# Kernel optimization log

Measured on AMD Instinct MI355X. Metric: run time of the kernel, lower is better.

Reference implementation:

```python
import jax, jax.numpy as jnp
import numpy as np

N, D, P = 8192, 512, 3
TEMP, SIM_TH, DIS_TH, CLIP = 0.1, 0.15, 0.35, 30.0
NEG = -1e9  # finite stand-in for -inf mask (exp underflows to 0 identically)


def setup_inputs() -> dict:
    key = jax.random.key(0)
    k1, k2 = jax.random.split(key)
    embeddings = jax.random.normal(k1, (N, D), dtype=jnp.float32)
    thetas = jax.random.uniform(k2, (N, P), dtype=jnp.float32)
    return {"embeddings": embeddings, "thetas": thetas}


def reference(embeddings, thetas):
    n = embeddings.shape[0]
    # F.normalize(dim=-1)
    e = embeddings / jnp.maximum(
        jnp.linalg.norm(embeddings, axis=-1, keepdims=True), 1e-12)
    sim = jnp.clip(e @ e.T / TEMP, -CLIP, CLIP)  # [N, N]

    # cdist(thetas, thetas) normalized by its max; only feeds boolean masks
    t = jax.lax.stop_gradient(thetas)
    sq = jnp.sum(t * t, axis=1)
    d2 = jnp.maximum(sq[:, None] + sq[None, :] - 2.0 * (t @ t.T), 0.0)
    dist = jnp.sqrt(d2)
    dist = dist / (dist.max() + 1e-8)

    eye = jnp.eye(n, dtype=bool)
    pos = (dist < SIM_TH) & ~eye      # positives (self excluded: diag is -inf masked)
    neg = dist > DIS_TH               # negatives (diag never included: dist==0)
    sel = pos | neg

    # per-row cross_entropy over logits [pos_idx; neg_idx] with label 0 is:
    #   -sim[i, first_pos_index(i)] + logsumexp_{j in sel(i)} sim[i, j]
    masked = jnp.where(sel, sim, NEG)
    denom = jax.nn.logsumexp(masked, axis=1)            # [N]
    tgt = jnp.argmax(pos, axis=1)                       # first positive index
    tgt_logit = jnp.take_along_axis(sim, tgt[:, None], axis=1)[:, 0]
    valid = pos.any(axis=1) & neg.any(axis=1)
    per_row = jnp.where(valid, denom - tgt_logit, 0.0)
    cnt = valid.sum()
    return jnp.where(cnt > 0, per_row.sum() / jnp.maximum(cnt, 1), 0.0)
```

## Files before the change

### kernel.cpp

```cpp
#include <hip/hip_runtime.h>

#define N 8192
#define D 512

typedef __attribute__((ext_vector_type(4))) float f32x4;
typedef __attribute__((ext_vector_type(2))) long long2v;

typedef const __attribute__((address_space(1))) unsigned int* gas_t;
typedef __attribute__((address_space(3))) unsigned int* las_t;

static __device__ __forceinline__ void gl_lds16(const void* g, char* l) {
    __builtin_amdgcn_global_load_lds((gas_t)g, (las_t)l, 16, 0, 0);
}
static __device__ __forceinline__ int tri_cum(int r) { return r * (129 - r) / 2; }

static __device__ __forceinline__ unsigned f2fp8(float f) {
    unsigned u = __float_as_uint(f);
    unsigned sgn = (u >> 24) & 0x80u;
    unsigned a = u & 0x7FFFFFFFu;
    if (a >= 0x3C800000u) {
        unsigned t = a + 0x7FFFFu + ((a >> 20) & 1u);
        unsigned code = (((t >> 23) - 120u) << 3) | ((t >> 20) & 7u);
        if (code > 0x7Eu) code = 0x7Eu;
        return sgn | code;
    }
    float af = __uint_as_float(a);
    unsigned m = (unsigned)(af * 512.0f + 0.5f);
    return sgn | (m > 8u ? 8u : m);
}
static __device__ __forceinline__ float fp82f(unsigned c) {
    unsigned e = (c >> 3) & 15u, m = c & 7u;
    float v = (e == 0u) ? (float)m * 0.001953125f
                        : __uint_as_float(((e + 120u) << 23) | (m << 20));
    return (c & 0x80u) ? -v : v;
}

__global__ void kpack(const float* __restrict__ th, float4* __restrict__ th4,
                      float* __restrict__ srow, unsigned* __restrict__ jminrow,
                      unsigned* __restrict__ negrow, unsigned* __restrict__ d2mb) {
    int i = blockIdx.x * 256 + threadIdx.x;
    if (i < N) {
        float x = th[3 * i], y = th[3 * i + 1], z = th[3 * i + 2];
        float4 v; v.x = x; v.y = y; v.z = z; v.w = x * x + y * y + z * z;
        th4[i] = v;
        srow[i] = 0.0f;
        jminrow[i] = 0xFFFFFFFFu;
        negrow[i] = 0u;
    }
    if (i == 0) *d2mb = 0u;
}

__global__ void knorm(const float* __restrict__ emb, unsigned char* __restrict__ e,
                      const float4* __restrict__ th4, unsigned* __restrict__ d2mb) {
    int w    = threadIdx.x >> 6;
    int row  = blockIdx.x * 4 + w;
    int lane = threadIdx.x & 63;
    const float4* src = (const float4*)(emb + (size_t)row * D);
    float4 v0 = src[lane * 2];
    float4 v1 = src[lane * 2 + 1];
    float ss = v0.x*v0.x + v0.y*v0.y + v0.z*v0.z + v0.w*v0.w
             + v1.x*v1.x + v1.y*v1.y + v1.z*v1.z + v1.w*v1.w;
#pragma unroll
    for (int off = 1; off < 64; off <<= 1) ss += __shfl_xor(ss, off, 64);
    float inv = 3.7982826f / fmaxf(sqrtf(ss), 1e-12f);
    unsigned c0 = f2fp8(v0.x * inv), c1 = f2fp8(v0.y * inv);
    unsigned c2 = f2fp8(v0.z * inv), c3 = f2fp8(v0.w * inv);
    unsigned c4 = f2fp8(v1.x * inv), c5 = f2fp8(v1.y * inv);
    unsigned c6 = f2fp8(v1.z * inv), c7 = f2fp8(v1.w * inv);
    uint2 pk;
    pk.x = c0 | (c1 << 8) | (c2 << 16) | (c3 << 24);
    pk.y = c4 | (c5 << 8) | (c6 << 16) | (c7 << 24);
    {
        int c = lane >> 3, u = lane & 7;
        int off8 = c * 64 + ((u < 4) ? u * 16 : (u - 4) * 16 + 8);
        *(uint2*)(e + (size_t)row * D + off8) = pk;
    }

    if (blockIdx.x < 256) {
        int widx = blockIdx.x * 4 + w;
        int q0 = widx * 4;
        int m0 = N - 4 - q0;
        float4 a0 = th4[q0], a1 = th4[q0 + 1], a2 = th4[q0 + 2], a3 = th4[q0 + 3];
        float4 b0 = th4[m0], b1 = th4[m0 + 1], b2 = th4[m0 + 2], b3 = th4[m0 + 3];
        float m = 0.0f;
        for (int j = q0 + 1 + lane; j < N; j += 64) {
            float4 tj = th4[j];
            float d;
            d = a0.w + tj.w - 2.0f * (a0.x*tj.x + a0.y*tj.y + a0.z*tj.z); m = fmaxf(m, d);
            d = a1.w + tj.w - 2.0f * (a1.x*tj.x + a1.y*tj.y + a1.z*tj.z); m = fmaxf(m, d);
            d = a2.w + tj.w - 2.0f * (a2.x*tj.x + a2.y*tj.y + a2.z*tj.z); m = fmaxf(m, d);
            d = a3.w + tj.w - 2.0f * (a3.x*tj.x + a3.y*tj.y + a3.z*tj.z); m = fmaxf(m, d);
        }
        for (int j = m0 + 1 + lane; j < N; j += 64) {
            float4 tj = th4[j];
            float d;
            d = b0.w + tj.w - 2.0f * (b0.x*tj.x + b0.y*tj.y + b0.z*tj.z); m = fmaxf(m, d);
            d = b1.w + tj.w - 2.0f * (b1.x*tj.x + b1.y*tj.y + b1.z*tj.z); m = fmaxf(m, d);
            d = b2.w + tj.w - 2.0f * (b2.x*tj.x + b2.y*tj.y + b2.z*tj.z); m = fmaxf(m, d);
            d = b3.w + tj.w - 2.0f * (b3.x*tj.x + b3.y*tj.y + b3.z*tj.z); m = fmaxf(m, d);
        }
#pragma unroll
        for (int off = 1; off < 64; off <<= 1) m = fmaxf(m, __shfl_xor(m, off, 64));
        if (lane == 0) atomicMax(d2mb, __float_as_uint(m));
    }
}

__global__ __launch_bounds__(256) void kmain(
    const unsigned char* __restrict__ e, const float4* __restrict__ th4,
    const unsigned* __restrict__ d2mb, float* __restrict__ srow,
    unsigned* __restrict__ jminrow, unsigned* __restrict__ negrow) {
    __shared__ __align__(16) char smem[32768];

    const int tid  = threadIdx.x;
    const int lane = tid & 63;
    const int w    = tid >> 6;
    const int wr   = w >> 1;
    const int wc   = w & 1;

    const int bid = (int)blockIdx.x;
    const int swz = (bid & 7) * 260 + (bid >> 3);
    int rb = (int)((129.0f - sqrtf(16641.0f - 8.0f * (float)swz)) * 0.5f);
    rb = rb < 0 ? 0 : (rb > 63 ? 63 : rb);
    while (tri_cum(rb + 1) <= swz) rb++;
    while (tri_cum(rb) > swz) rb--;
    const int cb = rb + (swz - tri_cum(rb));
    const bool isdiag = (rb == cb);
    const int r0 = rb * 128, c0 = cb * 128;

    const int ssw = (((tid & 3) ^ ((tid >> 3) & 3)) << 4);
    const unsigned char* pA0 = e + (size_t)(r0 + (tid >> 2)) * D + ssw;
    const unsigned char* pA1 = pA0 + (size_t)64 * D;
    const unsigned char* pB0 = e + (size_t)(c0 + (tid >> 2)) * D + ssw;
    const unsigned char* pB1 = pB0 + (size_t)64 * D;

    const int fr = lane & 15;
    const int fq = lane >> 4;
    const int kslot = (fq ^ ((fr >> 1) & 3)) << 4;

    f32x4 acc[4][4];
#pragma unroll
    for (int mt = 0; mt < 4; mt++)
#pragma unroll
        for (int nt = 0; nt < 4; nt++) acc[mt][nt] = (f32x4){0.f, 0.f, 0.f, 0.f};

#define STAGE(T, BUF) { \
    const int k0_ = (T) * 64; char* d_ = smem + (BUF) * 16384;   \
    gl_lds16(pA0 + k0_, d_ + tid * 16);                          \
    gl_lds16(pA1 + k0_, d_ + 4096 + tid * 16);                   \
    gl_lds16(pB0 + k0_, d_ + 8192 + tid * 16);                   \
    gl_lds16(pB1 + k0_, d_ + 12288 + tid * 16); }

#define COMPUTE(BUF) { \
    const char* cA_ = smem + (BUF) * 16384;                      \
    const char* cB_ = cA_ + 8192;                                \
    long2v a_[4], b_[4];                                         \
    _Pragma("unroll")                                            \
    for (int mt = 0; mt < 4; mt++)                               \
        a_[mt] = *(const long2v*)(cA_ + (wr * 64 + mt * 16 + fr) * 64 + kslot); \
    _Pragma("unroll")                                            \
    for (int nt = 0; nt < 4; nt++)                               \
        b_[nt] = *(const long2v*)(cB_ + (wc * 64 + nt * 16 + fr) * 64 + kslot); \
    _Pragma("unroll")                                            \
    for (int mt = 0; mt < 4; mt++)                               \
    _Pragma("unroll")                                            \
    for (int nt = 0; nt < 4; nt++) {                             \
        acc[mt][nt] = __builtin_amdgcn_mfma_f32_16x16x32_fp8_fp8( \
            a_[mt][0], b_[nt][0], acc[mt][nt], 0, 0, 0);         \
        acc[mt][nt] = __builtin_amdgcn_mfma_f32_16x16x32_fp8_fp8( \
            a_[mt][1], b_[nt][1], acc[mt][nt], 0, 0, 0);         \
    } }

#define KST(T)                                                    \
    if ((T) + 1 < 8) STAGE((T) + 1, ((T) + 1) & 1)                \
    COMPUTE((T) & 1)                                              \
    asm volatile("s_waitcnt vmcnt(0)" ::: "memory");              \
    __builtin_amdgcn_s_barrier();                                 \
    __builtin_amdgcn_sched_barrier(0);

    STAGE(0, 0)
    asm volatile("s_waitcnt vmcnt(0)" ::: "memory");
    __builtin_amdgcn_s_barrier();
    __builtin_amdgcn_sched_barrier(0);
    KST(0)  KST(1)  KST(2)  KST(3)
    KST(4)  KST(5)  KST(6)  KST(7)
#undef KST
#undef COMPUTE
#undef STAGE
    __syncthreads();

    const float dmax = sqrtf(__uint_as_float(*d2mb)) + 1e-8f;
    const float p2 = 0.0225f * dmax * dmax;
    const float n2 = 0.1225f * dmax * dmax;

    const int j0 = c0 + wc * 64 + fr;
    float4 thj[4];
#pragma unroll
    for (int nt = 0; nt < 4; nt++) thj[nt] = th4[j0 + nt * 16];

    float*    lds_rs = (float*)smem;
    unsigned* lds_rj = (unsigned*)(smem + 1024);
    unsigned* lds_rn = (unsigned*)(smem + 2048);
    float*    lds_cs = (float*)(smem + 3072);
    unsigned* lds_cj = (unsigned*)(smem + 4096);
    unsigned* lds_cn = (unsigned*)(smem + 5120);

    float    csum[4]; unsigned cjm[4], cng[4];
#pragma unroll
    for (int nt = 0; nt < 4; nt++) { csum[nt] = 0.0f; cjm[nt] = 0xFFFFFFFFu; cng[nt] = 0u; }

    const int i0 = r0 + wr * 64 + fq * 4;
#pragma unroll
    for (int mt = 0; mt < 4; mt++) {
#pragma unroll
        for (int rr = 0; rr < 4; rr++) {
            const int i = i0 + mt * 16 + rr;
            const float4 ti = th4[i];
            float sv = 0.0f; unsigned jv = 0xFFFFFFFFu, nv = 0u;
#pragma unroll
            for (int nt = 0; nt < 4; nt++) {
                const int j = j0 + nt * 16;
                const float4 tj = thj[nt];
                float dot = ti.x * tj.x + ti.y * tj.y + ti.z * tj.z;
                float d2 = fmaf(-2.0f, dot, ti.w + tj.w);
                bool pos = isdiag ? ((d2 < p2) && (j != i)) : (d2 < p2);
                bool neg = (d2 > n2);
                float c = (pos || neg) ? exp2f(acc[mt][nt][rr]) : 0.0f;
                sv += c;
                if (neg) nv = 1u;
                if (pos) jv = min(jv, (unsigned)j);
                if (!isdiag) {
                    csum[nt] += c;
                    if (neg) cng[nt] = 1u;
                    if (pos) cjm[nt] = min(cjm[nt], (unsigned)i);
                }
            }
#pragma unroll
            for (int off = 1; off < 16; off <<= 1) {
                sv += __shfl_xor(sv, off, 64);
                jv = min(jv, (unsigned)__shfl_xor((int)jv, off, 64));
                nv |= (unsigned)__shfl_xor((int)nv, off, 64);
            }
            if (fr == 0) {
                const int rl = wr * 64 + mt * 16 + fq * 4 + rr;
                lds_rs[wc * 128 + rl] = sv;
                lds_rj[wc * 128 + rl] = jv;
                lds_rn[wc * 128 + rl] = nv;
            }
        }
    }

    if (!isdiag) {
#pragma unroll
        for (int nt = 0; nt < 4; nt++) {
            float sv = csum[nt]; unsigned jv = cjm[nt], nv = cng[nt];
#pragma unroll
            for (int off = 16; off < 64; off <<= 1) {
                sv += __shfl_xor(sv, off, 64);
                jv = min(jv, (unsigned)__shfl_xor((int)jv, off, 64));
                nv |= (unsigned)__shfl_xor((int)nv, off, 64);
            }
            if (fq == 0) {
                const int cl = wc * 64 + nt * 16 + fr;
                lds_cs[wr * 128 + cl] = sv;
                lds_cj[wr * 128 + cl] = jv;
                lds_cn[wr * 128 + cl] = nv;
            }
        }
    }
    __syncthreads();
    if (tid < 128) {
        float    sv = lds_rs[tid] + lds_rs[128 + tid];
        unsigned jv = min(lds_rj[tid], lds_rj[128 + tid]);
        unsigned nv = lds_rn[tid] | lds_rn[128 + tid];
        atomicAdd(&srow[r0 + tid], sv);
        atomicMin(&jminrow[r0 + tid], jv);
        atomicOr(&negrow[r0 + tid], nv);
        if (!isdiag) {
            float    cv = lds_cs[tid] + lds_cs[128 + tid];
            unsigned cj = min(lds_cj[tid], lds_cj[128 + tid]);
            unsigned cn = lds_cn[tid] | lds_cn[128 + tid];
            atomicAdd(&srow[c0 + tid], cv);
            atomicMin(&jminrow[c0 + tid], cj);
            atomicOr(&negrow[c0 + tid], cn);
        }
    }
}

__global__ void krow(const unsigned char* __restrict__ e, const float* __restrict__ srow,
                     const unsigned* __restrict__ jminrow, const unsigned* __restrict__ negrow,
                     float* __restrict__ pr, float* __restrict__ vf) {
    int row  = blockIdx.x * 4 + (threadIdx.x >> 6);
    int lane = threadIdx.x & 63;
    unsigned jmv = jminrow[row];
    bool valid = (jmv != 0xFFFFFFFFu) && (negrow[row] != 0u);
    float p = 0.0f;
    if (valid) {
        const uint2* a = (const uint2*)(e + (size_t)row * D);
        const uint2* b = (const uint2*)(e + (size_t)jmv * D);
        uint2 va = a[lane], vb = b[lane];
        float dot = 0.0f;
#pragma unroll
        for (int k = 0; k < 4; k++)
            dot += fp82f((va.x >> (8 * k)) & 0xFFu) * fp82f((vb.x >> (8 * k)) & 0xFFu);
#pragma unroll
        for (int k = 0; k < 4; k++)
            dot += fp82f((va.y >> (8 * k)) & 0xFFu) * fp82f((vb.y >> (8 * k)) & 0xFFu);
#pragma unroll
        for (int off = 1; off < 64; off <<= 1) dot += __shfl_xor(dot, off, 64);
        p = logf(srow[row]) - dot * 0.69314718f;
    }
    if (lane == 0) { pr[row] = p; vf[row] = valid ? 1.0f : 0.0f; }
}

__global__ void kfinal(const float* __restrict__ pr, const float* __restrict__ vf,
                       float* __restrict__ out) {
    __shared__ float ls[1024];
    __shared__ float lc[1024];
    int t = threadIdx.x;
    float sv = 0.0f, cv = 0.0f;
#pragma unroll
    for (int k = 0; k < 8; k++) { sv += pr[t * 8 + k]; cv += vf[t * 8 + k]; }
    ls[t] = sv; lc[t] = cv;
    __syncthreads();
    for (int off = 512; off > 0; off >>= 1) {
        if (t < off) { ls[t] += ls[t + off]; lc[t] += lc[t + off]; }
        __syncthreads();
    }
    if (t == 0) out[0] = (lc[0] > 0.0f) ? (ls[0] / lc[0]) : 0.0f;
}

extern "C" void kernel_launch(void* const* d_in, const int* in_sizes, int n_in,
                              void* d_out, int out_size, void* d_ws, size_t ws_size,
                              hipStream_t stream) {
    const float* emb = (const float*)d_in[0];
    const float* th  = (const float*)d_in[1];
    float* out = (float*)d_out;
    char* ws = (char*)d_ws;

    unsigned char* e     = (unsigned char*)(ws);
    float4*   th4        = (float4*)(ws + 8388608);
    float*    srow       = (float*)(ws + 8519680);
    unsigned* jminr      = (unsigned*)(ws + 8552448);
    unsigned* negr       = (unsigned*)(ws + 8585216);
    float*    pr         = (float*)(ws + 8617984);
    float*    vf         = (float*)(ws + 8650752);
    unsigned* d2mb       = (unsigned*)(ws + 8683520);

    kpack<<<32, 256, 0, stream>>>(th, th4, srow, jminr, negr, d2mb);
    knorm<<<N / 4, 256, 0, stream>>>(emb, e, th4, d2mb);
    kmain<<<2080, 256, 0, stream>>>(e, th4, d2mb, srow, jminr, negr);
    krow<<<N / 4, 256, 0, stream>>>(e, srow, jminr, negr, pr, vf);
    kfinal<<<1, 1024, 0, stream>>>(pr, vf, out);
}
```

Before: 112.3 us.

## Triple-buffer GEMM K-loop and split theta max-distance pass into its own kernel

```diff
diff --git a/kernel.cpp b/kernel.cpp
--- a/kernel.cpp
+++ b/kernel.cpp
@@ -35,23 +35,9 @@
     return (c & 0x80u) ? -v : v;
 }
 
-__global__ void kpack(const float* __restrict__ th, float4* __restrict__ th4,
+__global__ void knorm(const float* __restrict__ emb, unsigned char* __restrict__ e,
                       float* __restrict__ srow, unsigned* __restrict__ jminrow,
                       unsigned* __restrict__ negrow, unsigned* __restrict__ d2mb) {
-    int i = blockIdx.x * 256 + threadIdx.x;
-    if (i < N) {
-        float x = th[3 * i], y = th[3 * i + 1], z = th[3 * i + 2];
-        float4 v; v.x = x; v.y = y; v.z = z; v.w = x * x + y * y + z * z;
-        th4[i] = v;
-        srow[i] = 0.0f;
-        jminrow[i] = 0xFFFFFFFFu;
-        negrow[i] = 0u;
-    }
-    if (i == 0) *d2mb = 0u;
-}
-
-__global__ void knorm(const float* __restrict__ emb, unsigned char* __restrict__ e,
-                      const float4* __restrict__ th4, unsigned* __restrict__ d2mb) {
     int w    = threadIdx.x >> 6;
     int row  = blockIdx.x * 4 + w;
     int lane = threadIdx.x & 63;
@@ -75,33 +61,62 @@
         int off8 = c * 64 + ((u < 4) ? u * 16 : (u - 4) * 16 + 8);
         *(uint2*)(e + (size_t)row * D + off8) = pk;
     }
-
-    if (blockIdx.x < 256) {
-        int widx = blockIdx.x * 4 + w;
-        int q0 = widx * 4;
-        int m0 = N - 4 - q0;
-        float4 a0 = th4[q0], a1 = th4[q0 + 1], a2 = th4[q0 + 2], a3 = th4[q0 + 3];
-        float4 b0 = th4[m0], b1 = th4[m0 + 1], b2 = th4[m0 + 2], b3 = th4[m0 + 3];
-        float m = 0.0f;
-        for (int j = q0 + 1 + lane; j < N; j += 64) {
-            float4 tj = th4[j];
-            float d;
-            d = a0.w + tj.w - 2.0f * (a0.x*tj.x + a0.y*tj.y + a0.z*tj.z); m = fmaxf(m, d);
-            d = a1.w + tj.w - 2.0f * (a1.x*tj.x + a1.y*tj.y + a1.z*tj.z); m = fmaxf(m, d);
-            d = a2.w + tj.w - 2.0f * (a2.x*tj.x + a2.y*tj.y + a2.z*tj.z); m = fmaxf(m, d);
-            d = a3.w + tj.w - 2.0f * (a3.x*tj.x + a3.y*tj.y + a3.z*tj.z); m = fmaxf(m, d);
-        }
-        for (int j = m0 + 1 + lane; j < N; j += 64) {
-            float4 tj = th4[j];
-            float d;
-            d = b0.w + tj.w - 2.0f * (b0.x*tj.x + b0.y*tj.y + b0.z*tj.z); m = fmaxf(m, d);
-            d = b1.w + tj.w - 2.0f * (b1.x*tj.x + b1.y*tj.y + b1.z*tj.z); m = fmaxf(m, d);
-            d = b2.w + tj.w - 2.0f * (b2.x*tj.x + b2.y*tj.y + b2.z*tj.z); m = fmaxf(m, d);
-            d = b3.w + tj.w - 2.0f * (b3.x*tj.x + b3.y*tj.y + b3.z*tj.z); m = fmaxf(m, d);
-        }
-#pragma unroll
-        for (int off = 1; off < 64; off <<= 1) m = fmaxf(m, __shfl_xor(m, off, 64));
-        if (lane == 0) atomicMax(d2mb, __float_as_uint(m));
+    if (lane == 0) {
+        srow[row] = 0.0f;
+        jminrow[row] = 0xFFFFFFFFu;
+        negrow[row] = 0u;
+    }
+    if (blockIdx.x == 0 && threadIdx.x == 0) *d2mb = 0u;
+}
+
+__global__ void kth(const float* __restrict__ th, float4* __restrict__ th4,
+                    unsigned* __restrict__ d2mb) {
+    int tid = threadIdx.x, bid = blockIdx.x;
+    if (bid < 32) {
+        int i = bid * 256 + tid;
+        float x = th[3 * i], y = th[3 * i + 1], z = th[3 * i + 2];
+        float4 v; v.x = x; v.y = y; v.z = z; v.w = x * x + y * y + z * z;
+        th4[i] = v;
+    }
+    int w = tid >> 6, lane = tid & 63;
+    int widx = bid * 4 + w;
+    int q0 = widx * 4;
+    int m0 = N - 4 - q0;
+    float4 A[4], B[4];
+#pragma unroll
+    for (int k = 0; k < 4; k++) {
+        float x = th[3 * (q0 + k)], y = th[3 * (q0 + k) + 1], z = th[3 * (q0 + k) + 2];
+        A[k].x = x; A[k].y = y; A[k].z = z; A[k].w = x * x + y * y + z * z;
+        x = th[3 * (m0 + k)]; y = th[3 * (m0 + k) + 1]; z = th[3 * (m0 + k) + 2];
+        B[k].x = x; B[k].y = y; B[k].z = z; B[k].w = x * x + y * y + z * z;
+    }
+    float m = 0.0f;
+    for (int j = q0 + 1 + lane; j < N; j += 64) {
+        float x = th[3 * j], y = th[3 * j + 1], z = th[3 * j + 2];
+        float tw = x * x + y * y + z * z;
+        float d;
+        d = A[0].w + tw - 2.0f * (A[0].x*x + A[0].y*y + A[0].z*z); m = fmaxf(m, d);
+        d = A[1].w + tw - 2.0f * (A[1].x*x + A[1].y*y + A[1].z*z); m = fmaxf(m, d);
+        d = A[2].w + tw - 2.0f * (A[2].x*x + A[2].y*y + A[2].z*z); m = fmaxf(m, d);
+        d = A[3].w + tw - 2.0f * (A[3].x*x + A[3].y*y + A[3].z*z); m = fmaxf(m, d);
+    }
+    for (int j = m0 + 1 + lane; j < N; j += 64) {
+        float x = th[3 * j], y = th[3 * j + 1], z = th[3 * j + 2];
+        float tw = x * x + y * y + z * z;
+        float d;
+        d = B[0].w + tw - 2.0f * (B[0].x*x + B[0].y*y + B[0].z*z); m = fmaxf(m, d);
+        d = B[1].w + tw - 2.0f * (B[1].x*x + B[1].y*y + B[1].z*z); m = fmaxf(m, d);
+        d = B[2].w + tw - 2.0f * (B[2].x*x + B[2].y*y + B[2].z*z); m = fmaxf(m, d);
+        d = B[3].w + tw - 2.0f * (B[3].x*x + B[3].y*y + B[3].z*z); m = fmaxf(m, d);
+    }
+#pragma unroll
+    for (int off = 1; off < 64; off <<= 1) m = fmaxf(m, __shfl_xor(m, off, 64));
+    __shared__ float red[4];
+    if (lane == 0) red[w] = m;
+    __syncthreads();
+    if (tid == 0) {
+        m = fmaxf(fmaxf(red[0], red[1]), fmaxf(red[2], red[3]));
+        atomicMax(d2mb, __float_as_uint(m));
     }
 }
 
@@ -109,7 +124,7 @@
     const unsigned char* __restrict__ e, const float4* __restrict__ th4,
     const unsigned* __restrict__ d2mb, float* __restrict__ srow,
     unsigned* __restrict__ jminrow, unsigned* __restrict__ negrow) {
-    __shared__ __align__(16) char smem[32768];
+    __shared__ __align__(16) char smem[49152];
 
     const int tid  = threadIdx.x;
     const int lane = tid & 63;
@@ -170,19 +185,23 @@
             a_[mt][1], b_[nt][1], acc[mt][nt], 0, 0, 0);         \
     } }
 
-#define KST(T)                                                    \
-    if ((T) + 1 < 8) STAGE((T) + 1, ((T) + 1) & 1)                \
-    COMPUTE((T) & 1)                                              \
-    asm volatile("s_waitcnt vmcnt(0)" ::: "memory");              \
+#define KST(WAITN, SBUF, DOSTAGE, ST, CBUF)                       \
+    asm volatile("s_waitcnt vmcnt(" #WAITN ")" ::: "memory");     \
     __builtin_amdgcn_s_barrier();                                 \
-    __builtin_amdgcn_sched_barrier(0);
+    __builtin_amdgcn_sched_barrier(0);                            \
+    if (DOSTAGE) STAGE(ST, SBUF)                                  \
+    COMPUTE(CBUF)
 
     STAGE(0, 0)
-    asm volatile("s_waitcnt vmcnt(0)" ::: "memory");
-    __builtin_amdgcn_s_barrier();
-    __builtin_amdgcn_sched_barrier(0);
-    KST(0)  KST(1)  KST(2)  KST(3)
-    KST(4)  KST(5)  KST(6)  KST(7)
+    STAGE(1, 1)
+    KST(4, 2, 1, 2, 0)
+    KST(4, 0, 1, 3, 1)
+    KST(4, 1, 1, 4, 2)
+    KST(4, 2, 1, 5, 0)
+    KST(4, 0, 1, 6, 1)
+    KST(4, 1, 1, 7, 2)
+    KST(4, 0, 0, 0, 0)
+    KST(0, 0, 0, 0, 1)
 #undef KST
 #undef COMPUTE
 #undef STAGE
@@ -346,8 +365,8 @@
     float*    vf         = (float*)(ws + 8650752);
     unsigned* d2mb       = (unsigned*)(ws + 8683520);
 
-    kpack<<<32, 256, 0, stream>>>(th, th4, srow, jminr, negr, d2mb);
-    knorm<<<N / 4, 256, 0, stream>>>(emb, e, th4, d2mb);
+    knorm<<<N / 4, 256, 0, stream>>>(emb, e, srow, jminr, negr, d2mb);
+    kth<<<256, 256, 0, stream>>>(th, th4, d2mb);
     kmain<<<2080, 256, 0, stream>>>(e, th4, d2mb, srow, jminr, negr);
     krow<<<N / 4, 256, 0, stream>>>(e, srow, jminr, negr, pr, vf);
     kfinal<<<1, 1024, 0, stream>>>(pr, vf, out);
```

Result: no change. 110.9 us (median of 3 runs) (-1.2%).
